# Performance work log

Hardware: AMD Instinct MI355X
Metric: run time of the kernel (lower is better)

## Reference

```python
import jax, jax.numpy as jnp
import numpy as np

B, S, DIM, HD = 4, 1024, 2048, 128
H = DIM // HD  # 16 heads
GN_EPS = 1e-3  # Keras GroupNormalization default epsilon


def setup_inputs() -> dict:
    key = jax.random.key(0)
    ks = jax.random.split(key, 8)
    x = jax.random.normal(ks[0], (B, S, DIM), dtype=jnp.float32)
    k = jax.random.normal(ks[1], (B, S, DIM), dtype=jnp.float32)
    v = jax.random.normal(ks[2], (B, S, DIM), dtype=jnp.float32)
    # One shared QKV projection weight per head (dict.fromkeys bug in source
    # makes Q, K, V use the SAME Dense layer). Keras Dense: y = x @ W, W:(in,out)
    Wh = jax.random.normal(ks[3], (H, HD, HD), dtype=jnp.float32) / np.sqrt(HD)
    wg_w = jax.random.normal(ks[4], (DIM, DIM), dtype=jnp.float32) / np.sqrt(DIM)
    wo_w = jax.random.normal(ks[5], (DIM, DIM), dtype=jnp.float32) / np.sqrt(DIM)
    gn_gamma = jnp.ones((DIM,), dtype=jnp.float32)
    gn_beta = jnp.zeros((DIM,), dtype=jnp.float32)
    return {"x": x, "k": k, "v": v, "Wh": Wh, "wg_w": wg_w, "wo_w": wo_w,
            "gn_gamma": gn_gamma, "gn_beta": gn_beta}


def _decay_masks(n_heads, seq_len):
    # Source: band_part(gamma**(i-j), 0, -1) then transpose ->
    # D[h, i, j] = gamma_h ** (j - i) for j <= i, else 0.
    gam = 1.0 - 2.0 ** (-5.0 - jnp.arange(n_heads, dtype=jnp.float32))  # (H,)
    idx = jnp.arange(seq_len, dtype=jnp.float32)
    expo = idx[None, :] - idx[:, None]               # (S,S): j - i
    D = jnp.where(expo[None, :, :] <= 0,
                  gam[:, None, None] ** expo[None, :, :], 0.0)  # (H,S,S)
    # TF: D /= reduce_sum(D, 1)**0.5 broadcasts row-sums along the COLUMN axis
    return D / jnp.sqrt(D.sum(axis=-1))[:, None, :]


def reference(x, k, v, Wh, wg_w, wo_w, gn_gamma, gn_beta):
    b, s, dim = x.shape
    h, hd, _ = Wh.shape
    # split last axis into contiguous per-head chunks
    xh = x.reshape(b, s, h, hd)
    kh = k.reshape(b, s, h, hd)
    vh = v.reshape(b, s, h, hd)
    # Q, K, V share the same per-head weight (faithful to dict.fromkeys)
    Q = jnp.einsum('bshd,hde->bshe', xh, Wh)
    K = jnp.einsum('bshd,hde->bshe', kh, Wh)
    V = jnp.einsum('bshd,hde->bshe', vh, Wh)
    scores = jnp.einsum('bshe,bthe->bhst', Q, K) / jnp.sqrt(jnp.float32(hd))
    Dn = _decay_masks(h, s)                          # (H,S,S)
    masked = scores * Dn[None, :, :, :]              # (B,H,S,S)
    # source reduces over axis 0 == BATCH, then abs, then clamp at 1
    A = jnp.maximum(jnp.abs(masked.sum(axis=0)), 1.0)  # (H,S,S)
    O = jnp.einsum('hst,bthe->bshe', A, V).reshape(b, s, dim)
    # GroupNormalization(groups=1): per-token layernorm over channels
    mu = O.mean(axis=-1, keepdims=True)
    var = O.var(axis=-1, keepdims=True)
    Y = (O - mu) / jnp.sqrt(var + GN_EPS) * gn_gamma + gn_beta
    W = jax.nn.relu(x @ wg_w)                        # gated branch
    return (W * Y) @ wo_w
```

## Files before the change

### kernel.cpp

```cpp
#include <hip/hip_runtime.h>
#include <math.h>

constexpr int Bc = 4, Sc = 1024, Dc = 2048, HDc = 128, Hc = 16;
constexpr int BSc = Bc * Sc;
constexpr int KQKc = Bc * HDc;
#define GN_EPS 1e-3f

typedef __bf16 bf16x8 __attribute__((ext_vector_type(8)));
typedef __bf16 bf16x4 __attribute__((ext_vector_type(4)));
typedef float f32x4 __attribute__((ext_vector_type(4)));

constexpr size_t OFF_Q   = 0;
constexpr size_t OFF_K   = OFF_Q + (size_t)Hc * Sc * KQKc / 2;
constexpr size_t OFF_VB  = OFF_K + (size_t)Hc * Sc * KQKc / 2;
constexpr size_t OFF_VT  = OFF_VB + (size_t)BSc * Dc / 2;
constexpr size_t OFF_A   = OFF_VT + (size_t)BSc * Dc / 2;
constexpr size_t OFF_O   = OFF_A + (size_t)Hc * Sc * Sc / 2;
constexpr size_t OFF_CT  = OFF_O + (size_t)BSc * Dc;
constexpr size_t OFF_PN  = OFF_CT + (size_t)Hc * Sc;
constexpr size_t OFF_XB  = OFF_PN + (size_t)Hc * Sc;
constexpr size_t OFF_WGT = OFF_XB + (size_t)BSc * Dc / 2;
constexpr size_t OFF_WOT = OFF_WGT + (size_t)Dc * Dc / 2;
constexpr size_t OFF_SUF = OFF_WOT + (size_t)Dc * Dc / 2;
constexpr size_t OFF_T   = OFF_SUF + (size_t)64 * 9 * HDc;
constexpr size_t OFF_WHT = OFF_T + (size_t)64 * 8 * HDc;
constexpr size_t OFF_STAT= OFF_WHT + (size_t)Hc * HDc * HDc / 2;
constexpr size_t OFF_KB2 = OFF_A;
constexpr size_t OFF_VB2 = OFF_A + (size_t)BSc * Dc / 2;

#define GLOAD_LDS16(gp, lp)                                               \
  __builtin_amdgcn_global_load_lds(                                       \
      (const __attribute__((address_space(1))) void*)(gp),                \
      (__attribute__((address_space(3))) void*)(lp), 16, 0, 0)


constexpr int ABUFE = 128 * 64;
constexpr int BBUFE = 128 * 64;
constexpr int MG_LDS = (3 * ABUFE + 2 * BBUFE) * 2;
constexpr int PJ_LDS = 4 * 8192 * 2;
constexpr int AV_LDS = (3 * 64 * 64 + 2 * BBUFE) * 2;

template <int ASTR, int BSTR, int NF = 4, int MF = 4>
__device__ __forceinline__ void mfma_loop128(const __bf16* __restrict__ Abase,
                                             const __bf16* __restrict__ Bbase,
                                             const int ntk,
                                             __bf16* As, __bf16* Bs,
                                             const int wave, const int lane,
                                             f32x4 acc[MF][NF]) {
  constexpr int NH = NF / 2;
  constexpr int MH = MF / 2;
  constexpr int ABE = MF * 2048;
  const int wr = wave >> 1, wc = wave & 1;
  const int lr = lane >> 2;
  const int lkx = ((lane & 3) ^ ((lane >> 3) & 3)) * 8;
  const int rl = lane & 15, kq = lane >> 4;
  const int swo = rl * 32 + ((kq ^ ((rl >> 1) & 3)) * 8);

#define VMW_MF()                                                            \
  do {                                                                      \
    if constexpr (MF == 4)                                                  \
      asm volatile("s_waitcnt vmcnt(4)" ::: "memory");                      \
    else                                                                    \
      asm volatile("s_waitcnt vmcnt(2)" ::: "memory");                      \
  } while (0)

#define SA_(i, kt, bsel) do {                                               \
    const int ci_ = (i) * 4 + wave;                                         \
    GLOAD_LDS16(Abase + (size_t)((ci_ >> 1) * 16 + lr) * ASTR               \
                    + (kt) * 64 + (ci_ & 1) * 32 + lkx,                     \
                As + (bsel) * ABE + ci_ * 512);                             \
  } while (0)
#define SB_(j, kt, bsel) do {                                               \
    const int ci_ = (j) * 4 + wave;                                         \
    GLOAD_LDS16(Bbase + (size_t)((ci_ >> 1) * 16 + lr) * BSTR               \
                    + (kt) * 64 + (ci_ & 1) * 32 + lkx,                     \
                Bs + (bsel) * BBUFE + ci_ * 512);                           \
  } while (0)

  #pragma unroll
  for (int i = 0; i < MF; ++i) SA_(i, 0, 0);
  #pragma unroll
  for (int j = 0; j < NF; ++j) SB_(j, 0, 0);
  #pragma unroll
  for (int i = 0; i < MF; ++i) SA_(i, 1, 1);
  __builtin_amdgcn_sched_barrier(0);
  VMW_MF();
  __builtin_amdgcn_sched_barrier(0);
  __builtin_amdgcn_s_barrier();

  int cbA = 0;
  for (int t = 0; t < ntk; ++t) {
    const int sbA = (cbA + 2 >= 3) ? cbA - 1 : cbA + 2;
    const __bf16* Ac = As + cbA * ABE;
    const __bf16* Bc = Bs + (t & 1) * BBUFE;
    bf16x8 a[MF][2], b[NF][2];
    #pragma unroll
    for (int m = 0; m < MH; ++m)
      #pragma unroll
      for (int kc = 0; kc < 2; ++kc)
        a[m][kc] = *(const bf16x8*)&Ac[((wr * MF + m) * 2 + kc) * 512 + swo];
    #pragma unroll
    for (int n = 0; n < NH; ++n)
      #pragma unroll
      for (int kc = 0; kc < 2; ++kc)
        b[n][kc] = *(const bf16x8*)&Bc[((wc * NF + n) * 2 + kc) * 512 + swo];
    #pragma unroll
    for (int m = MH; m < MF; ++m)
      #pragma unroll
      for (int kc = 0; kc < 2; ++kc)
        a[m][kc] = *(const bf16x8*)&Ac[((wr * MF + m) * 2 + kc) * 512 + swo];
    #pragma unroll
    for (int n = NH; n < NF; ++n)
      #pragma unroll
      for (int kc = 0; kc < 2; ++kc)
        b[n][kc] = *(const bf16x8*)&Bc[((wc * NF + n) * 2 + kc) * 512 + swo];
    if (t + 1 < ntk) {
      #pragma unroll
      for (int j = 0; j < NF; ++j) SB_(j, t + 1, (t + 1) & 1);
    }
    if (t + 2 < ntk) {
      #pragma unroll
      for (int i = 0; i < MF; ++i) SA_(i, t + 2, sbA);
    }
    __builtin_amdgcn_sched_barrier(0);
    __builtin_amdgcn_s_setprio(1);
    #pragma unroll
    for (int kc = 0; kc < 2; ++kc)
      #pragma unroll
      for (int m = 0; m < MH; ++m)
        #pragma unroll
        for (int n = 0; n < NH; ++n)
          acc[m][n] = __builtin_amdgcn_mfma_f32_16x16x32_bf16(
              a[m][kc], b[n][kc], acc[m][n], 0, 0, 0);
    __builtin_amdgcn_s_setprio(0);
    __builtin_amdgcn_sched_barrier(0);
    __builtin_amdgcn_s_setprio(1);
    #pragma unroll
    for (int kc = 0; kc < 2; ++kc)
      #pragma unroll
      for (int m = MH; m < MF; ++m)
        #pragma unroll
        for (int n = 0; n < NH; ++n)
          acc[m][n] = __builtin_amdgcn_mfma_f32_16x16x32_bf16(
              a[m][kc], b[n][kc], acc[m][n], 0, 0, 0);
    __builtin_amdgcn_s_setprio(0);
    __builtin_amdgcn_sched_barrier(0);
    __builtin_amdgcn_s_setprio(1);
    #pragma unroll
    for (int kc = 0; kc < 2; ++kc)
      #pragma unroll
      for (int m = 0; m < MH; ++m)
        #pragma unroll
        for (int n = NH; n < NF; ++n)
          acc[m][n] = __builtin_amdgcn_mfma_f32_16x16x32_bf16(
              a[m][kc], b[n][kc], acc[m][n], 0, 0, 0);
    __builtin_amdgcn_s_setprio(0);
    __builtin_amdgcn_sched_barrier(0);
    __builtin_amdgcn_s_setprio(1);
    #pragma unroll
    for (int kc = 0; kc < 2; ++kc)
      #pragma unroll
      for (int m = MH; m < MF; ++m)
        #pragma unroll
        for (int n = NH; n < NF; ++n)
          acc[m][n] = __builtin_amdgcn_mfma_f32_16x16x32_bf16(
              a[m][kc], b[n][kc], acc[m][n], 0, 0, 0);
    __builtin_amdgcn_s_setprio(0);
    __builtin_amdgcn_sched_barrier(0);
    asm volatile("s_waitcnt lgkmcnt(0)" ::: "memory");
    __builtin_amdgcn_sched_barrier(0);
    if (t + 2 < ntk) {
      VMW_MF();
    } else if (t + 1 < ntk) {
      asm volatile("s_waitcnt vmcnt(0)" ::: "memory");
    }
    __builtin_amdgcn_sched_barrier(0);
    __builtin_amdgcn_s_barrier();
    cbA = (cbA + 1 >= 3) ? 0 : cbA + 1;
  }
#undef SA_
#undef SB_
#undef VMW_MF
}

__global__ __launch_bounds__(256) void k_tables(float* __restrict__ ct,
                                                float* __restrict__ pn,
                                                float* __restrict__ TP,
                                                float* __restrict__ STAT) {
  int idx = blockIdx.x * 256 + threadIdx.x;
  int h = idx >> 10, t = idx & 1023;
  double gamma = 1.0 - exp2(-(double)(5 + h));
  double l2g = log2(gamma);
  double r = 1.0 / gamma;
  double rowsum = (exp2(-(double)(t + 1) * l2g) - 1.0) / (r - 1.0);
  ct[idx] = (float)(exp2((double)t * l2g) / sqrt(rowsum));
  pn[idx] = (float)exp2(-(double)t * l2g);
  float4 z4 = {0.f, 0.f, 0.f, 0.f};
  *(float4*)(TP + (size_t)idx * 4) = z4;
  if (idx < BSc * 2) STAT[idx] = 0.f;
}

__global__ __launch_bounds__(256) void k_cast83(const float* __restrict__ s0,
                                                const float* __restrict__ s1,
                                                const float* __restrict__ s2,
                                                __bf16* __restrict__ d0,
                                                __bf16* __restrict__ d1,
                                                __bf16* __restrict__ d2) {
  const int y = blockIdx.y;
  const float* src = (y == 0) ? s0 : (y == 1) ? s1 : s2;
  __bf16* dst = (y == 0) ? d0 : (y == 1) ? d1 : d2;
  size_t i = ((size_t)blockIdx.x * 256 + threadIdx.x) * 8;
  float4 a = *(const float4*)(src + i);
  float4 b = *(const float4*)(src + i + 4);
  bf16x8 o;
  o[0] = (__bf16)a.x; o[1] = (__bf16)a.y; o[2] = (__bf16)a.z; o[3] = (__bf16)a.w;
  o[4] = (__bf16)b.x; o[5] = (__bf16)b.y; o[6] = (__bf16)b.z; o[7] = (__bf16)b.w;
  *(bf16x8*)(dst + i) = o;
}

__global__ __launch_bounds__(256) void k_castT2(const float* __restrict__ s0,
                                                const float* __restrict__ s1,
                                                __bf16* __restrict__ d0,
                                                __bf16* __restrict__ d1) {
  __shared__ float t[32][33];
  const int bx = blockIdx.x, by = blockIdx.y;
  const float* src = blockIdx.z ? s1 : s0;
  __bf16* dst = blockIdx.z ? d1 : d0;
  const int tid = threadIdx.x;
  const int lx = tid & 31, ly = tid >> 5;
  #pragma unroll
  for (int r = 0; r < 32; r += 8)
    t[ly + r][lx] = src[(size_t)(by * 32 + ly + r) * Dc + bx * 32 + lx];
  __syncthreads();
  #pragma unroll
  for (int r = 0; r < 32; r += 8)
    dst[(size_t)(bx * 32 + ly + r) * Dc + by * 32 + lx] = (__bf16)t[lx][ly + r];
}

__global__ __launch_bounds__(256) void k_whT(const float* __restrict__ Wh,
                                             __bf16* __restrict__ WhT) {
  __shared__ float t[32][33];
  const int h = blockIdx.z;
  const int d0 = blockIdx.x * 32, e0 = blockIdx.y * 32;
  const int tid = threadIdx.x;
  const int lx = tid & 31, ly = tid >> 5;
  #pragma unroll
  for (int r = 0; r < 32; r += 8)
    t[ly + r][lx] = Wh[(size_t)h * HDc * HDc + (d0 + ly + r) * HDc + e0 + lx];
  __syncthreads();
  #pragma unroll
  for (int r = 0; r < 32; r += 8)
    WhT[(size_t)h * HDc * HDc + (e0 + ly + r) * HDc + d0 + lx] =
        (__bf16)t[lx][ly + r];
}

__global__ __launch_bounds__(256, 2) void k_projm(const __bf16* __restrict__ Xb,
                                                  const __bf16* __restrict__ Kb2,
                                                  const __bf16* __restrict__ Vb2,
                                                  const __bf16* __restrict__ WhT,
                                                  __bf16* __restrict__ Qo,
                                                  __bf16* __restrict__ Ko,
                                                  __bf16* __restrict__ Vo) {
  extern __shared__ __bf16 lds[];
  __bf16* Xs = lds;
  __bf16* Ws = lds + 2 * 8192;
  const int r0 = blockIdx.x * 128;
  const int h = blockIdx.y;
  const int z = blockIdx.z;
  const __bf16* src = (z == 0) ? Xb : (z == 1) ? Kb2 : Vb2;
  const __bf16* wsrc = WhT + (size_t)h * HDc * HDc;
  const int tid = threadIdx.x;
  const int wave = tid >> 6, lane = tid & 63;
  const int wr = wave >> 1, wc = wave & 1;
  const int lr = lane >> 2;
  const int lkx = ((lane & 3) ^ ((lane >> 3) & 3)) * 8;
  const int rl = lane & 15, kq = lane >> 4;
  const int swo = rl * 32 + ((kq ^ ((rl >> 1) & 3)) * 8);
  #pragma unroll
  for (int kt = 0; kt < 2; ++kt) {
    #pragma unroll
    for (int i = 0; i < 4; ++i) {
      const int ci = i * 4 + wave;
      const int row = (ci >> 1) * 16 + lr;
      const int ko = kt * 64 + (ci & 1) * 32 + lkx;
      GLOAD_LDS16(src + (size_t)(r0 + row) * Dc + h * HDc + ko,
                  Xs + kt * 8192 + ci * 512);
      GLOAD_LDS16(wsrc + (size_t)row * HDc + ko, Ws + kt * 8192 + ci * 512);
    }
  }
  __builtin_amdgcn_sched_barrier(0);
  asm volatile("s_waitcnt vmcnt(0)" ::: "memory");
  __builtin_amdgcn_sched_barrier(0);
  __builtin_amdgcn_s_barrier();
  f32x4 acc[4][4] = {{}};
  #pragma unroll
  for (int kt = 0; kt < 2; ++kt) {
    bf16x8 a[4][2], b[4][2];
    #pragma unroll
    for (int m = 0; m < 4; ++m)
      #pragma unroll
      for (int kc = 0; kc < 2; ++kc)
        a[m][kc] =
            *(const bf16x8*)&Xs[kt * 8192 + ((wr * 4 + m) * 2 + kc) * 512 + swo];
    #pragma unroll
    for (int n = 0; n < 4; ++n)
      #pragma unroll
      for (int kc = 0; kc < 2; ++kc)
        b[n][kc] =
            *(const bf16x8*)&Ws[kt * 8192 + ((wc * 4 + n) * 2 + kc) * 512 + swo];
    #pragma unroll
    for (int kc = 0; kc < 2; ++kc)
      #pragma unroll
      for (int m = 0; m < 4; ++m)
        #pragma unroll
        for (int n = 0; n < 4; ++n)
          acc[m][n] = __builtin_amdgcn_mfma_f32_16x16x32_bf16(
              a[m][kc], b[n][kc], acc[m][n], 0, 0, 0);
  }
  #pragma unroll
  for (int mi = 0; mi < 4; ++mi) {
    #pragma unroll
    for (int nj = 0; nj < 4; ++nj) {
      const int col = wc * 64 + nj * 16 + rl;
      #pragma unroll
      for (int r = 0; r < 4; ++r) {
        const int row = r0 + wr * 64 + mi * 16 + kq * 4 + r;
        const __bf16 v = (__bf16)acc[mi][nj][r];
        if (z == 2) {
          Vo[(size_t)row * Dc + h * HDc + col] = v;
        } else {
          const int s = row & 1023, bb = row >> 10;
          __bf16* dst = (z == 0) ? Qo : Ko;
          dst[((size_t)(h * Sc + s) * Bc + bb) * HDc + col] = v;
        }
      }
    }
  }
}

__global__ __launch_bounds__(256) void k_vt(const __bf16* __restrict__ VB,
                                            __bf16* __restrict__ Vt,
                                            float* __restrict__ TP) {
  __shared__ float tl[32][33];
  __shared__ float rs[8][32];
  const int bh = blockIdx.z, bb = bh >> 4, h = bh & 15;
  const int t0 = blockIdx.x * 32, e0 = blockIdx.y * 32;
  const int tid = threadIdx.x;
  const int lx = tid & 31, ly = tid >> 5;
  float ps = 0.f;
  #pragma unroll
  for (int r = 0; r < 32; r += 8) {
    const float v =
        (float)VB[(size_t)(bb * Sc + t0 + ly + r) * Dc + h * HDc + e0 + lx];
    tl[ly + r][lx] = v;
    ps += v;
  }
  rs[ly][lx] = ps;
  __syncthreads();
  #pragma unroll
  for (int r = 0; r < 32; r += 8)
    Vt[((size_t)bh * HDc + e0 + ly + r) * Sc + t0 + lx] = (__bf16)tl[lx][ly + r];
  if (ly == 0) {
    float s = ((rs[0][lx] + rs[1][lx]) + (rs[2][lx] + rs[3][lx])) +
              ((rs[4][lx] + rs[5][lx]) + (rs[6][lx] + rs[7][lx]));
    atomicAdd(&TP[((size_t)bh * 8 + (t0 >> 7)) * HDc + e0 + lx], s);
  }
}

__global__ __launch_bounds__(128) void k_vscan(const float* __restrict__ T,
                                               float* __restrict__ SufV) {
  const int bh = blockIdx.x;
  const int e = threadIdx.x;
  float acc = 0.f;
  SufV[((size_t)bh * 9 + 8) * HDc + e] = 0.f;
  for (int jj = 7; jj >= 1; --jj) {
    acc += T[((size_t)bh * 8 + jj) * HDc + e];
    SufV[((size_t)bh * 9 + jj) * HDc + e] = acc;
  }
}

__global__ __launch_bounds__(256, 2) void k_ssm(const __bf16* __restrict__ Q,
                                                const __bf16* __restrict__ Kb,
                                                const float* __restrict__ ct,
                                                const float* __restrict__ pn,
                                                __bf16* __restrict__ A) {
  const int bx = blockIdx.x, by = blockIdx.y;
  int r, c, half;
  if (by == 8)       { r = bx; c = bx; half = 1; }
  else if (bx > by)  { r = bx; c = by; half = 1; }
  else               { r = by; c = bx; half = 0; }
  extern __shared__ __bf16 lds[];
  __bf16* As = lds;
  __bf16* Bs = lds + 3 * ABUFE;
  const int h = blockIdx.z;
  const int s0 = r * 128;
  const int t0 = c * 128 + half * 64;
  const int tid = threadIdx.x;
  __bf16* Ah = A + (size_t)h * Sc * Sc;
  const int wave = tid >> 6, lane = tid & 63;
  f32x4 acc[4][2] = {{}};
  mfma_loop128<KQKc, KQKc, 2>(Q + (size_t)(h * Sc + s0) * KQKc,
                              Kb + (size_t)(h * Sc + t0) * KQKc, KQKc / 64,
                              As, Bs, wave, lane, acc);
  const int wr = wave >> 1, wc = wave & 1;
  const int rl = lane & 15, kq = lane >> 4;
  const float rs = 0.088388347648318447f;
  #pragma unroll
  for (int mi = 0; mi < 4; ++mi) {
    #pragma unroll
    for (int nj = 0; nj < 2; ++nj) {
      const int t = t0 + wc * 32 + nj * 16 + rl;
      const float ctv = ct[h * Sc + t] * rs;
      #pragma unroll
      for (int rr = 0; rr < 4; ++rr) {
        const int s = s0 + wr * 64 + mi * 16 + kq * 4 + rr;
        float v = 1.0f;
        if (t <= s) v = fmaxf(fabsf(ctv * pn[h * Sc + s] * acc[mi][nj][rr]), 1.0f);
        Ah[(size_t)s * Sc + t] = (__bf16)v;
      }
    }
  }
}

__global__ __launch_bounds__(256, 2) void k_avm(const __bf16* __restrict__ A,
                                                const __bf16* __restrict__ Vt,
                                                const float* __restrict__ SufV,
                                                float* __restrict__ O,
                                                float* __restrict__ STAT) {
  extern __shared__ __bf16 lds[];
  __bf16* As = lds;
  __bf16* Bs = lds + 3 * 64 * 64;
  const int bh = blockIdx.z, bb = bh >> 4, h = bh & 15;
  const int j = (int)blockIdx.x >> 1;
  const int hh0 = (int)blockIdx.x & 1;
  const int tid = threadIdx.x;
  const int wave = tid >> 6, lane = tid & 63;
  const int wr = wave >> 1, wc = wave & 1;
  const int rl = lane & 15, kq = lane >> 4;
  #pragma unroll
  for (int seg = 0; seg < 2; ++seg) {
    const int itile = seg ? 7 - j : j;
    const int hh = seg ? 1 - hh0 : hh0;
    const int s0 = itile * 128 + hh * 64;
    f32x4 acc[2][4] = {{}};
    mfma_loop128<Sc, Sc, 4, 2>(A + (size_t)(h * Sc + s0) * Sc,
                               Vt + (size_t)bh * HDc * Sc, (itile + 1) * 2,
                               As, Bs, wave, lane, acc);
    const float* sufr = SufV + ((size_t)bh * 9 + (itile + 1)) * HDc;
    #pragma unroll
    for (int mi = 0; mi < 2; ++mi) {
      #pragma unroll
      for (int r = 0; r < 4; ++r) {
        const int s = s0 + wr * 32 + mi * 16 + kq * 4 + r;
        const size_t orow = (size_t)(bb * Sc + s);
        float vs = 0.f, vq = 0.f;
        #pragma unroll
        for (int nj = 0; nj < 4; ++nj) {
          const int e = wc * 64 + nj * 16 + rl;
          const float v = acc[mi][nj][r] + sufr[e];
          O[orow * Dc + h * HDc + e] = v;
          vs += v;
          vq += v * v;
        }
        #pragma unroll
        for (int m = 1; m < 16; m <<= 1) {
          vs += __shfl_xor(vs, m);
          vq += __shfl_xor(vq, m);
        }
        if (rl == 0) {
          atomicAdd(&STAT[orow * 2], vs);
          atomicAdd(&STAT[orow * 2 + 1], vq);
        }
      }
    }
  }
}

__global__ __launch_bounds__(256, 2) void k_mgemm(const __bf16* __restrict__ Ab,
                                                  const __bf16* __restrict__ Bt,
                                                  const float* __restrict__ Y,
                                                  const float* __restrict__ gw,
                                                  const float* __restrict__ bw,
                                                  const float* __restrict__ STAT,
                                                  __bf16* __restrict__ Gout,
                                                  float* __restrict__ Fout,
                                                  int mode) {
  extern __shared__ __bf16 lds[];
  __bf16* As = lds;
  __bf16* Bs = lds + 3 * ABUFE;
  int wid = blockIdx.y * gridDim.x + blockIdx.x;
  wid = (wid & 7) * 64 + (wid >> 3);
  const int r0 = (wid >> 4) * 128;
  const int c0 = (wid & 15) * 128;
  const int tid = threadIdx.x;
  const int wave = tid >> 6, lane = tid & 63;
  f32x4 acc[4][4] = {{}};
  mfma_loop128<Dc, Dc>(Ab + (size_t)r0 * Dc, Bt + (size_t)c0 * Dc, Dc / 64,
                       As, Bs, wave, lane, acc);
  const int wr = wave >> 1, wc = wave & 1;
  const int rl = lane & 15, kq = lane >> 4;
  if (mode == 0) {
    #pragma unroll
    for (int mi = 0; mi < 4; ++mi) {
      #pragma unroll
      for (int r = 0; r < 4; ++r) {
        const int row = r0 + wr * 64 + mi * 16 + kq * 4 + r;
        const float mu = STAT[(size_t)row * 2] * (1.0f / Dc);
        const float va = STAT[(size_t)row * 2 + 1] * (1.0f / Dc) - mu * mu;
        const float inv = rsqrtf(va + GN_EPS);
        #pragma unroll
        for (int nj = 0; nj < 4; ++nj) {
          const int col = c0 + wc * 64 + nj * 16 + rl;
          const size_t idx = (size_t)row * Dc + col;
          const float yv = (Y[idx] - mu) * inv * gw[col] + bw[col];
          Gout[idx] = (__bf16)(fmaxf(acc[mi][nj][r], 0.f) * yv);
        }
      }
    }
  } else {
    #pragma unroll
    for (int mi = 0; mi < 4; ++mi) {
      #pragma unroll
      for (int nj = 0; nj < 4; ++nj) {
        const int col = c0 + wc * 64 + nj * 16 + rl;
        #pragma unroll
        for (int r = 0; r < 4; ++r) {
          const int row = r0 + wr * 64 + mi * 16 + kq * 4 + r;
          Fout[(size_t)row * Dc + col] = acc[mi][nj][r];
        }
      }
    }
  }
}

extern "C" void kernel_launch(void* const* d_in, const int* in_sizes, int n_in,
                              void* d_out, int out_size, void* d_ws, size_t ws_size,
                              hipStream_t stream) {
  const float* x  = (const float*)d_in[0];
  const float* k  = (const float*)d_in[1];
  const float* v  = (const float*)d_in[2];
  const float* Wh = (const float*)d_in[3];
  const float* wg = (const float*)d_in[4];
  const float* wo = (const float*)d_in[5];
  const float* gg = (const float*)d_in[6];
  const float* gb = (const float*)d_in[7];
  float* ws = (float*)d_ws;
  __bf16* Q   = (__bf16*)(ws + OFF_Q);
  __bf16* Kp  = (__bf16*)(ws + OFF_K);
  __bf16* VB  = (__bf16*)(ws + OFF_VB);
  __bf16* Vt  = (__bf16*)(ws + OFF_VT);
  __bf16* A   = (__bf16*)(ws + OFF_A);
  float*  O   = ws + OFF_O;
  float*  CT  = ws + OFF_CT;
  float*  PN  = ws + OFF_PN;
  __bf16* XB  = (__bf16*)(ws + OFF_XB);
  __bf16* WGT = (__bf16*)(ws + OFF_WGT);
  __bf16* WOT = (__bf16*)(ws + OFF_WOT);
  float*  SUF = ws + OFF_SUF;
  float*  TP  = ws + OFF_T;
  __bf16* WHT = (__bf16*)(ws + OFF_WHT);
  float*  STAT= ws + OFF_STAT;
  __bf16* KB2 = (__bf16*)(ws + OFF_KB2);
  __bf16* VB2 = (__bf16*)(ws + OFF_VB2);
  __bf16* G   = (__bf16*)(ws + OFF_Q);

  static bool attr_done = false;
  if (!attr_done) {
    (void)hipFuncSetAttribute((const void*)k_mgemm,
                              hipFuncAttributeMaxDynamicSharedMemorySize,
                              MG_LDS);
    (void)hipFuncSetAttribute((const void*)k_projm,
                              hipFuncAttributeMaxDynamicSharedMemorySize,
                              PJ_LDS);
    (void)hipFuncSetAttribute((const void*)k_ssm,
                              hipFuncAttributeMaxDynamicSharedMemorySize,
                              MG_LDS);
    (void)hipFuncSetAttribute((const void*)k_avm,
                              hipFuncAttributeMaxDynamicSharedMemorySize,
                              AV_LDS);
    attr_done = true;
  }

  k_tables<<<Hc * Sc / 256, 256, 0, stream>>>(CT, PN, TP, STAT);
  k_cast83<<<dim3((BSc * Dc) / (256 * 8), 3), 256, 0, stream>>>(
      x, k, v, XB, KB2, VB2);
  k_castT2<<<dim3(Dc / 32, Dc / 32, 2), 256, 0, stream>>>(wg, wo, WGT, WOT);
  k_whT<<<dim3(4, 4, Hc), 256, 0, stream>>>(Wh, WHT);
  k_projm<<<dim3(BSc / 128, Hc, 3), 256, PJ_LDS, stream>>>(XB, KB2, VB2, WHT,
                                                           Q, Kp, VB);
  k_vt<<<dim3(Sc / 32, HDc / 32, Bc * Hc), 256, 0, stream>>>(VB, Vt, TP);
  k_vscan<<<Bc * Hc, 128, 0, stream>>>(TP, SUF);
  k_ssm<<<dim3(8, 9, Hc), 256, MG_LDS, stream>>>(Q, Kp, CT, PN, A);
  k_avm<<<dim3(8, 1, Bc * Hc), 256, AV_LDS, stream>>>(A, Vt, SUF, O, STAT);
  k_mgemm<<<dim3(16, 32), 256, MG_LDS, stream>>>(XB, WGT, O, gg, gb, STAT, G,
                                                 nullptr, 0);
  k_mgemm<<<dim3(16, 32), 256, MG_LDS, stream>>>(G, WOT, nullptr, nullptr,
                                                 nullptr, nullptr, nullptr,
                                                 (float*)d_out, 1);
}
```

Before: 365.2 us.

## Fuse V transpose and column sums into projection; retile AV GEMM to 128-row tiles

```diff
diff --git a/kernel.cpp b/kernel.cpp
--- a/kernel.cpp
+++ b/kernel.cpp
@@ -38,7 +38,6 @@
 constexpr int BBUFE = 128 * 64;
 constexpr int MG_LDS = (3 * ABUFE + 2 * BBUFE) * 2;
 constexpr int PJ_LDS = 4 * 8192 * 2;
-constexpr int AV_LDS = (3 * 64 * 64 + 2 * BBUFE) * 2;
 
 template <int ASTR, int BSTR, int NF = 4, int MF = 4>
 __device__ __forceinline__ void mfma_loop128(const __bf16* __restrict__ Abase,
@@ -260,7 +259,8 @@
                                                   const __bf16* __restrict__ WhT,
                                                   __bf16* __restrict__ Qo,
                                                   __bf16* __restrict__ Ko,
-                                                  __bf16* __restrict__ Vo) {
+                                                  __bf16* __restrict__ Vt,
+                                                  float* __restrict__ TP) {
   extern __shared__ __bf16 lds[];
   __bf16* Xs = lds;
   __bf16* Ws = lds + 2 * 8192;
@@ -317,53 +317,53 @@
           acc[m][n] = __builtin_amdgcn_mfma_f32_16x16x32_bf16(
               a[m][kc], b[n][kc], acc[m][n], 0, 0, 0);
   }
-  #pragma unroll
-  for (int mi = 0; mi < 4; ++mi) {
-    #pragma unroll
-    for (int nj = 0; nj < 4; ++nj) {
-      const int col = wc * 64 + nj * 16 + rl;
-      #pragma unroll
-      for (int r = 0; r < 4; ++r) {
-        const int row = r0 + wr * 64 + mi * 16 + kq * 4 + r;
-        const __bf16 v = (__bf16)acc[mi][nj][r];
-        if (z == 2) {
-          Vo[(size_t)row * Dc + h * HDc + col] = v;
-        } else {
+  if (z == 2) {
+    __bf16* tl = lds;
+    __syncthreads();
+    #pragma unroll
+    for (int mi = 0; mi < 4; ++mi) {
+      #pragma unroll
+      for (int nj = 0; nj < 4; ++nj) {
+        const int col = wc * 64 + nj * 16 + rl;
+        const int rrb = wr * 64 + mi * 16 + kq * 4;
+        bf16x4 v4;
+        v4[0] = (__bf16)acc[mi][nj][0];
+        v4[1] = (__bf16)acc[mi][nj][1];
+        v4[2] = (__bf16)acc[mi][nj][2];
+        v4[3] = (__bf16)acc[mi][nj][3];
+        *(bf16x4*)&tl[col * 132 + rrb] = v4;
+      }
+    }
+    __syncthreads();
+    const int e = tid >> 1, rh = (tid & 1) * 64;
+    const int bh2 = (r0 >> 10) * 16 + h;
+    const int jj = (r0 & 1023) >> 7;
+    const int sb = r0 & 1023;
+    float colsum = 0.f;
+    #pragma unroll
+    for (int j = 0; j < 8; ++j) {
+      bf16x8 v = *(const bf16x8*)&tl[e * 132 + rh + j * 8];
+      #pragma unroll
+      for (int q = 0; q < 8; ++q) colsum += (float)v[q];
+      *(bf16x8*)&Vt[((size_t)bh2 * HDc + e) * Sc + sb + rh + j * 8] = v;
+    }
+    atomicAdd(&TP[((size_t)bh2 * 8 + jj) * HDc + e], colsum);
+  } else {
+    __bf16* dst = (z == 0) ? Qo : Ko;
+    #pragma unroll
+    for (int mi = 0; mi < 4; ++mi) {
+      #pragma unroll
+      for (int nj = 0; nj < 4; ++nj) {
+        const int col = wc * 64 + nj * 16 + rl;
+        #pragma unroll
+        for (int r = 0; r < 4; ++r) {
+          const int row = r0 + wr * 64 + mi * 16 + kq * 4 + r;
           const int s = row & 1023, bb = row >> 10;
-          __bf16* dst = (z == 0) ? Qo : Ko;
-          dst[((size_t)(h * Sc + s) * Bc + bb) * HDc + col] = v;
+          dst[((size_t)(h * Sc + s) * Bc + bb) * HDc + col] =
+              (__bf16)acc[mi][nj][r];
         }
       }
     }
-  }
-}
-
-__global__ __launch_bounds__(256) void k_vt(const __bf16* __restrict__ VB,
-                                            __bf16* __restrict__ Vt,
-                                            float* __restrict__ TP) {
-  __shared__ float tl[32][33];
-  __shared__ float rs[8][32];
-  const int bh = blockIdx.z, bb = bh >> 4, h = bh & 15;
-  const int t0 = blockIdx.x * 32, e0 = blockIdx.y * 32;
-  const int tid = threadIdx.x;
-  const int lx = tid & 31, ly = tid >> 5;
-  float ps = 0.f;
-  #pragma unroll
-  for (int r = 0; r < 32; r += 8) {
-    const float v =
-        (float)VB[(size_t)(bb * Sc + t0 + ly + r) * Dc + h * HDc + e0 + lx];
-    tl[ly + r][lx] = v;
-    ps += v;
-  }
-  rs[ly][lx] = ps;
-  __syncthreads();
-  #pragma unroll
-  for (int r = 0; r < 32; r += 8)
-    Vt[((size_t)bh * HDc + e0 + ly + r) * Sc + t0 + lx] = (__bf16)tl[lx][ly + r];
-  if (ly == 0) {
-    float s = ((rs[0][lx] + rs[1][lx]) + (rs[2][lx] + rs[3][lx])) +
-              ((rs[4][lx] + rs[5][lx]) + (rs[6][lx] + rs[7][lx]));
-    atomicAdd(&TP[((size_t)bh * 8 + (t0 >> 7)) * HDc + e0 + lx], s);
   }
 }
 
@@ -429,48 +429,45 @@
                                                 float* __restrict__ STAT) {
   extern __shared__ __bf16 lds[];
   __bf16* As = lds;
-  __bf16* Bs = lds + 3 * 64 * 64;
-  const int bh = blockIdx.z, bb = bh >> 4, h = bh & 15;
-  const int j = (int)blockIdx.x >> 1;
-  const int hh0 = (int)blockIdx.x & 1;
+  __bf16* Bs = lds + 3 * ABUFE;
+  const int lid = (int)blockIdx.z * 8 + (int)blockIdx.x;
+  const int slot = lid & 255;
+  const int bh = slot >> 2;
+  const int itile = (lid < 256) ? (slot & 3) : 7 - (slot & 3);
+  const int bb = bh >> 4, h = bh & 15;
+  const int s0 = itile * 128;
   const int tid = threadIdx.x;
   const int wave = tid >> 6, lane = tid & 63;
   const int wr = wave >> 1, wc = wave & 1;
   const int rl = lane & 15, kq = lane >> 4;
-  #pragma unroll
-  for (int seg = 0; seg < 2; ++seg) {
-    const int itile = seg ? 7 - j : j;
-    const int hh = seg ? 1 - hh0 : hh0;
-    const int s0 = itile * 128 + hh * 64;
-    f32x4 acc[2][4] = {{}};
-    mfma_loop128<Sc, Sc, 4, 2>(A + (size_t)(h * Sc + s0) * Sc,
-                               Vt + (size_t)bh * HDc * Sc, (itile + 1) * 2,
-                               As, Bs, wave, lane, acc);
-    const float* sufr = SufV + ((size_t)bh * 9 + (itile + 1)) * HDc;
-    #pragma unroll
-    for (int mi = 0; mi < 2; ++mi) {
-      #pragma unroll
-      for (int r = 0; r < 4; ++r) {
-        const int s = s0 + wr * 32 + mi * 16 + kq * 4 + r;
-        const size_t orow = (size_t)(bb * Sc + s);
-        float vs = 0.f, vq = 0.f;
-        #pragma unroll
-        for (int nj = 0; nj < 4; ++nj) {
-          const int e = wc * 64 + nj * 16 + rl;
-          const float v = acc[mi][nj][r] + sufr[e];
-          O[orow * Dc + h * HDc + e] = v;
-          vs += v;
-          vq += v * v;
-        }
-        #pragma unroll
-        for (int m = 1; m < 16; m <<= 1) {
-          vs += __shfl_xor(vs, m);
-          vq += __shfl_xor(vq, m);
-        }
-        if (rl == 0) {
-          atomicAdd(&STAT[orow * 2], vs);
-          atomicAdd(&STAT[orow * 2 + 1], vq);
-        }
+  f32x4 acc[4][4] = {{}};
+  mfma_loop128<Sc, Sc>(A + (size_t)(h * Sc + s0) * Sc,
+                       Vt + (size_t)bh * HDc * Sc, (itile + 1) * 2, As, Bs,
+                       wave, lane, acc);
+  const float* sufr = SufV + ((size_t)bh * 9 + (itile + 1)) * HDc;
+  #pragma unroll
+  for (int mi = 0; mi < 4; ++mi) {
+    #pragma unroll
+    for (int r = 0; r < 4; ++r) {
+      const int s = s0 + wr * 64 + mi * 16 + kq * 4 + r;
+      const size_t orow = (size_t)(bb * Sc + s);
+      float vs = 0.f, vq = 0.f;
+      #pragma unroll
+      for (int nj = 0; nj < 4; ++nj) {
+        const int e = wc * 64 + nj * 16 + rl;
+        const float v = acc[mi][nj][r] + sufr[e];
+        O[orow * Dc + h * HDc + e] = v;
+        vs += v;
+        vq += v * v;
+      }
+      #pragma unroll
+      for (int m = 1; m < 16; m <<= 1) {
+        vs += __shfl_xor(vs, m);
+        vq += __shfl_xor(vq, m);
+      }
+      if (rl == 0) {
+        atomicAdd(&STAT[orow * 2], vs);
+        atomicAdd(&STAT[orow * 2 + 1], vq);
       }
     }
   }
@@ -547,7 +544,6 @@
   float* ws = (float*)d_ws;
   __bf16* Q   = (__bf16*)(ws + OFF_Q);
   __bf16* Kp  = (__bf16*)(ws + OFF_K);
-  __bf16* VB  = (__bf16*)(ws + OFF_VB);
   __bf16* Vt  = (__bf16*)(ws + OFF_VT);
   __bf16* A   = (__bf16*)(ws + OFF_A);
   float*  O   = ws + OFF_O;
@@ -577,7 +573,7 @@
                               MG_LDS);
     (void)hipFuncSetAttribute((const void*)k_avm,
                               hipFuncAttributeMaxDynamicSharedMemorySize,
-                              AV_LDS);
+                              MG_LDS);
     attr_done = true;
   }
 
@@ -587,11 +583,10 @@
   k_castT2<<<dim3(Dc / 32, Dc / 32, 2), 256, 0, stream>>>(wg, wo, WGT, WOT);
   k_whT<<<dim3(4, 4, Hc), 256, 0, stream>>>(Wh, WHT);
   k_projm<<<dim3(BSc / 128, Hc, 3), 256, PJ_LDS, stream>>>(XB, KB2, VB2, WHT,
-                                                           Q, Kp, VB);
-  k_vt<<<dim3(Sc / 32, HDc / 32, Bc * Hc), 256, 0, stream>>>(VB, Vt, TP);
+                                                           Q, Kp, Vt, TP);
   k_vscan<<<Bc * Hc, 128, 0, stream>>>(TP, SUF);
   k_ssm<<<dim3(8, 9, Hc), 256, MG_LDS, stream>>>(Q, Kp, CT, PN, A);
-  k_avm<<<dim3(8, 1, Bc * Hc), 256, AV_LDS, stream>>>(A, Vt, SUF, O, STAT);
+  k_avm<<<dim3(8, 1, Bc * Hc), 256, MG_LDS, stream>>>(A, Vt, SUF, O, STAT);
   k_mgemm<<<dim3(16, 32), 256, MG_LDS, stream>>>(XB, WGT, O, gg, gb, STAT, G,
                                                  nullptr, 0);
   k_mgemm<<<dim3(16, 32), 256, MG_LDS, stream>>>(G, WOT, nullptr, nullptr,
```

New measurement: 346.1 us. 5.2% less time.
